# Optimization experiments

Hardware: AMD Instinct MI355X
Metric: run time of the kernel (lower is better)

Reference implementation:

```python
import jax, jax.numpy as jnp
import numpy as np

GNN_NODES = 100000
D = 256          # hidden_channels / embed_dim
T = 4096         # tgt_len
B = 64           # bsz


def setup_inputs() -> dict:
    key = jax.random.key(0)
    k1, k2, k3, k4, k5, k6 = jax.random.split(key, 6)
    batch_nodes = jax.random.randint(k1, (B, T), 0, GNN_NODES, dtype=jnp.int64)
    batch_nodes_exe = jax.random.randint(k2, (B, T), 0, 2, dtype=jnp.int32)
    src = jax.random.normal(k3, (T, B, D), dtype=jnp.float32)
    # precomputed GNN node embeddings (self.graph_dict, detached)
    graph_dict = jax.random.normal(k4, (GNN_NODES, D), dtype=jnp.float32)
    # linear0 params
    W0 = jax.random.normal(k5, (D, D), dtype=jnp.float32) / np.sqrt(D)
    b0 = jax.random.normal(k6, (D,), dtype=jnp.float32) * 0.01
    return {"batch_nodes": batch_nodes, "batch_nodes_exe": batch_nodes_exe,
            "src": src, "graph_dict": graph_dict, "W0": W0, "b0": b0}


def reference(batch_nodes, batch_nodes_exe, src, graph_dict, W0, b0):
    tgt_len, bsz, embed_dim = src.shape
    # Vectorized last-occurrence-of-1 search (replaces the Python loop):
    pos = jnp.arange(tgt_len, dtype=jnp.int32)                      # [T]
    masked_pos = jnp.where(batch_nodes_exe == 1, pos[None, :], -1)  # [B,T]
    doc_id = jnp.max(masked_pos, axis=1)                            # [B], -1 if no 1
    has_one = doc_id >= 0                                           # [B]
    safe_doc = jnp.clip(doc_id, 0, tgt_len - 1)
    node_idx = jnp.take_along_axis(batch_nodes, safe_doc[:, None].astype(batch_nodes.dtype), axis=1)[:, 0]  # [B]
    gathered = graph_dict[node_idx]                                 # [B,D]
    new_x = jnp.where(has_one[:, None], gathered, 0.0)[:, None, :]  # [B,1,D]
    gate_x = has_one.astype(src.dtype)[:, None]                     # [B,1]
    # linear0
    x = jnp.einsum('bod,ed->boe', new_x, W0) + b0                   # [B,1,D]
    # scaled similarity: [B,1,D] @ [B,D,T] -> [B,1,T]
    scale = 1.0 / jnp.sqrt(jnp.asarray(embed_dim, dtype=jnp.float32))
    cosine_sim_matrix = jnp.einsum('bod,tbd->bot', x, src) * scale
    return (cosine_sim_matrix, gate_x)
```

## Files before the change

### kernel.cpp

```cpp
#include <hip/hip_runtime.h>

#define T 4096
#define B 64
#define D 256

__global__ __launch_bounds__(256) void prep_kernel(
    const int* __restrict__ batch_nodes, const int* __restrict__ exe,
    const float* __restrict__ graph_dict, const float* __restrict__ W0,
    const float* __restrict__ b0, float* __restrict__ x_ws,
    float* __restrict__ gate_out)
{
    const int b   = blockIdx.x;
    const int tid = threadIdx.x;

    int best = -1;
    const int* erow = exe + (size_t)b * T;
    for (int t = tid; t < T; t += 256)
        if (erow[t] == 1) best = t;

    for (int off = 32; off > 0; off >>= 1) {
        int o = __shfl_down(best, off, 64);
        best = best > o ? best : o;
    }
    __shared__ int sred[4];
    __shared__ int s_doc;
    const int wid = tid >> 6, lane = tid & 63;
    if (lane == 0) sred[wid] = best;
    __syncthreads();
    if (tid == 0) {
        int m = sred[0];
        if (sred[1] > m) m = sred[1];
        if (sred[2] > m) m = sred[2];
        if (sred[3] > m) m = sred[3];
        s_doc = m;
    }
    __syncthreads();

    const int  doc  = s_doc;
    const bool has  = doc >= 0;
    const int  safe = has ? doc : 0;
    const int  node = batch_nodes[(size_t)b * T + safe];

    __shared__ float s_g[D];
    s_g[tid] = has ? graph_dict[(size_t)node * D + tid] : 0.0f;
    __syncthreads();

    const int e = tid;
    const float4* wrow = (const float4*)(W0 + (size_t)e * D);
    float acc = b0[e];
    #pragma unroll 8
    for (int d4 = 0; d4 < D / 4; ++d4) {
        float4 w = wrow[d4];
        acc += s_g[d4 * 4 + 0] * w.x + s_g[d4 * 4 + 1] * w.y
             + s_g[d4 * 4 + 2] * w.z + s_g[d4 * 4 + 3] * w.w;
    }
    x_ws[(size_t)b * D + e] = acc;
    if (tid == 0) gate_out[b] = has ? 1.0f : 0.0f;
}

__global__ __launch_bounds__(256) void sim_kernel(
    const float* __restrict__ src, const float* __restrict__ x_ws,
    float* __restrict__ out)
{
    const int wave = (blockIdx.x << 2) | (threadIdx.x >> 6);
    const int lane = threadIdx.x & 63;
    const int b = wave >> 12;
    const int t = wave & (T - 1);

    const float4 xv = *(const float4*)(x_ws + (size_t)b * D + lane * 4);
    const float4 sv = *(const float4*)(src + (size_t)t * (B * D) + (size_t)b * D + lane * 4);

    float acc = xv.x * sv.x + xv.y * sv.y + xv.z * sv.z + xv.w * sv.w;
    for (int off = 32; off > 0; off >>= 1)
        acc += __shfl_down(acc, off, 64);

    if (lane == 0) out[(size_t)b * T + t] = acc * 0.0625f;
}

extern "C" void kernel_launch(void* const* d_in, const int* in_sizes, int n_in,
                              void* d_out, int out_size, void* d_ws, size_t ws_size,
                              hipStream_t stream) {
    const int*   batch_nodes = (const int*)d_in[0];
    const int*   exe         = (const int*)d_in[1];
    const float* src         = (const float*)d_in[2];
    const float* graph_dict  = (const float*)d_in[3];
    const float* W0          = (const float*)d_in[4];
    const float* b0          = (const float*)d_in[5];

    float* out    = (float*)d_out;
    float* gate   = out + (size_t)B * T;
    float* x_ws   = (float*)d_ws;

    prep_kernel<<<B, 256, 0, stream>>>(batch_nodes, exe, graph_dict, W0, b0, x_ws, gate);
    sim_kernel<<<(B * T) / 4, 256, 0, stream>>>(src, x_ws, out);
}
```

Measured before the change: 412.6 us.

## Process one time step per block with each wave handling sixteen batches

The similarity kernel now launches one block per time step instead of one wave per (batch, time) pair. Each wave loops over 16 batch rows, reading contiguous src memory, and finishes each dot product with an xor butterfly reduction. Each lane keeps one result, so a wave writes 16 outputs. This amortizes launch and per-wave overhead and gives more memory-level parallelism per wave, at the cost of more shuffle instructions and output writes strided by T.

```diff
diff --git a/kernel.cpp b/kernel.cpp
--- a/kernel.cpp
+++ b/kernel.cpp
@@ -62,19 +62,30 @@
     const float* __restrict__ src, const float* __restrict__ x_ws,
     float* __restrict__ out)
 {
-    const int wave = (blockIdx.x << 2) | (threadIdx.x >> 6);
+    const int t    = blockIdx.x;
+    const int wave = threadIdx.x >> 6;
     const int lane = threadIdx.x & 63;
-    const int b = wave >> 12;
-    const int t = wave & (T - 1);
+    const int b0   = wave * 16;
 
-    const float4 xv = *(const float4*)(x_ws + (size_t)b * D + lane * 4);
-    const float4 sv = *(const float4*)(src + (size_t)t * (B * D) + (size_t)b * D + lane * 4);
+    const float* srow = src  + (size_t)t * (B * D) + (size_t)b0 * D + lane * 4;
+    const float* xrow = x_ws + (size_t)b0 * D + lane * 4;
 
-    float acc = xv.x * sv.x + xv.y * sv.y + xv.z * sv.z + xv.w * sv.w;
-    for (int off = 32; off > 0; off >>= 1)
-        acc += __shfl_down(acc, off, 64);
-
-    if (lane == 0) out[(size_t)b * T + t] = acc * 0.0625f;
+    float res = 0.0f;
+    #pragma unroll
+    for (int i = 0; i < 16; ++i) {
+        const float4 sv = *(const float4*)(srow + i * D);
+        const float4 xv = *(const float4*)(xrow + i * D);
+        float a = sv.x * xv.x + sv.y * xv.y + sv.z * xv.z + sv.w * xv.w;
+        a += __shfl_xor(a, 1, 64);
+        a += __shfl_xor(a, 2, 64);
+        a += __shfl_xor(a, 4, 64);
+        a += __shfl_xor(a, 8, 64);
+        a += __shfl_xor(a, 16, 64);
+        a += __shfl_xor(a, 32, 64);
+        if (lane == i) res = a;
+    }
+    if (lane < 16)
+        out[(size_t)(b0 + lane) * T + t] = res * 0.0625f;
 }
 
 extern "C" void kernel_launch(void* const* d_in, const int* in_sizes, int n_in,
@@ -87,10 +98,10 @@
     const float* W0          = (const float*)d_in[4];
     const float* b0          = (const float*)d_in[5];
 
-    float* out    = (float*)d_out;
-    float* gate   = out + (size_t)B * T;
-    float* x_ws   = (float*)d_ws;
+    float* out  = (float*)d_out;
+    float* gate = out + (size_t)B * T;
+    float* x_ws = (float*)d_ws;
 
     prep_kernel<<<B, 256, 0, stream>>>(batch_nodes, exe, graph_dict, W0, b0, x_ws, gate);
-    sim_kernel<<<(B * T) / 4, 256, 0, stream>>>(src, x_ws, out);
+    sim_kernel<<<T, 256, 0, stream>>>(src, x_ws, out);
 }
```

Result: no change. 410.5 us (-0.5%).
